# Kernel tuning notes

Hardware: AMD Instinct MI355X
Metric: run time of the kernel (lower is better)

The kernel has to match this reference:

```python
import jax, jax.numpy as jnp
import numpy as np

B, E, N, NREL, K, T, L = 8, 2000, 10000, 25, 16, 3, 32
TAU1 = 10.0

def _clip01(x):
    return jnp.clip(x, 0.0, 1.0)

def setup_inputs():
    key = jax.random.key(0)
    ks = jax.random.split(key, 10)
    ent = jax.random.randint(ks[0], (B,), 0, E)
    input_x = jnp.zeros((B, E), jnp.float32).at[jnp.arange(B), ent].set(1.0)
    tidx = jax.random.randint(ks[1], (E,), 0, K)
    type_mat = jnp.zeros((E, K), jnp.float32).at[jnp.arange(E), tidx].set(1.0)
    heads = jax.random.randint(ks[2], (N,), 0, E)
    tails = jax.random.randint(ks[3], (N,), 0, E)
    rels = jax.random.randint(ks[4], (N,), 0, NREL)
    e2triple = jnp.zeros((E, N), jnp.float32).at[heads, jnp.arange(N)].set(1.0)
    triple2e = jnp.zeros((N, E), jnp.float32).at[jnp.arange(N), tails].set(1.0)
    triple2r = jnp.zeros((N, NREL), jnp.float32).at[jnp.arange(N), rels].set(1.0)
    def ku(k, shape):
        fan_in = int(np.prod(shape[1:]))
        bnd = 1.0 / np.sqrt(fan_in)
        return jax.random.uniform(k, shape, jnp.float32, -bnd, bnd)
    w = ku(ks[5], (T, L, NREL))
    weight = ku(ks[6], (L, 1))
    h = jnp.ones((T, L, NREL - 1), jnp.float32)
    h_x = jnp.ones((L, NREL - 1), jnp.float32)
    h_type = ku(ks[7], (T, L, K))
    h_x_type = ku(ks[8], (L, K))
    alpha = jnp.ones((T, L), jnp.float32)
    beta = jnp.ones((T, L), jnp.float32)
    alpha_x = jnp.ones((L,), jnp.float32)
    beta_x = jnp.ones((L,), jnp.float32)
    return dict(input_x=input_x, type_mat=type_mat, e2triple=e2triple,
                triple2e=triple2e, triple2r=triple2r, w=w, weight=weight,
                h=h, h_x=h_x, h_type=h_type, h_x_type=h_x_type,
                alpha=alpha, beta=beta, alpha_x=alpha_x, beta_x=beta_x, flag=0)

def _forward(input_x, type_mat, e2triple, triple2e, triple2r, w, weight,
             h, h_x, h_type, h_x_type, alpha, beta, alpha_x, beta_x):
    # flag=False, is_training=False path of TCLMModel.forward
    Bb = input_x.shape[0]
    Nn, Ee = triple2e.shape
    Tt, Ll = alpha.shape
    nrel = w.shape[-1]
    half = (nrel - 1) // 2
    x_ori = input_x @ e2triple                      # [B,N]
    e2r = triple2e.T @ triple2r                     # [E,nrel]
    hidden_base = _clip01(e2r)[:, :-1]              # [E,nrel-1]
    hx_raw = _clip01(x_ori @ triple2r)              # [B,nrel]
    hidden_x_base = jnp.concatenate([hx_raw[:, half:-1], hx_raw[:, :half]], axis=-1)
    ax = _clip01(alpha_x / TAU1)
    bx = _clip01(beta_x / TAU1)
    gate_x = 1.0 - _clip01(ax + bx)                 # [L]
    hxp = _clip01(h_x / TAU1)                       # [L,nrel-1]
    hxtp = _clip01(h_x_type / TAU1)                 # [L,K]
    hidden_type_x = input_x @ (type_mat @ hxtp.T)   # [B,L]
    hx_lin = hidden_x_base @ hxp.T                  # [B,L]
    s = None
    for t in range(Tt):
        a = _clip01(alpha[t] / TAU1)                # [L]
        b = _clip01(beta[t] / TAU1)
        hp = _clip01(h[t] / TAU1)                   # [L,nrel-1]
        htp = _clip01(h_type[t] / TAU1)             # [L,K]
        hidden = _clip01(a[None] * (type_mat @ htp.T) + b[None] * (hidden_base @ hp.T))
        hidden = (hidden + (1.0 - _clip01(a + b))[None]).T        # [L,E]
        # note: original code uses alpha/beta (not alpha_x/beta_x) here; replicate
        hidden_x = _clip01(a[None] * hidden_type_x + b[None] * hx_lin) + gate_x[None]  # [B,L]
        w_probs = jax.nn.softmax(w[t], axis=-1)     # [L,nrel]
        srel = triple2r @ w_probs.T                 # [N,L]
        if t == 0:
            sc = x_ori[:, None, :] * srel.T[None]   # [B,L,N]
            s = (sc.reshape(-1, Nn) @ triple2e).reshape(Bb, Ll, Ee)
            s = s * hidden[None] * hidden_x[:, :, None]
        else:
            xprev = (s.reshape(-1, Ee) @ e2triple).reshape(Bb, Ll, Nn)
            sc = xprev * srel.T[None]               # [B,L,N]
            s = (sc.reshape(-1, Nn) @ triple2e).reshape(Bb, Ll, Ee)
            s = s * hidden[None]
    out = jnp.einsum('ble,lk->bek', s, jnp.tanh(weight))[..., 0]  # [B,E]
    return out

def reference(input_x, type_mat, e2triple, triple2e, triple2r, w, weight,
              h, h_x, h_type, h_x_type, alpha, beta, alpha_x, beta_x, flag):
    return _forward(input_x, type_mat, e2triple, triple2e, triple2r, w, weight,
                    h, h_x, h_type, h_x_type, alpha, beta, alpha_x, beta_x)
```

## Files before the change

### kernel.cpp

```cpp
#include <hip/hip_runtime.h>

#define B 8
#define E 2000
#define NTRI 10000
#define NRELS 25
#define KT 16
#define TT 3
#define LL 32
#define TAU1 10.0f
#define XBLK 2048
#define XTHR 256

__device__ __forceinline__ float clip01(float x) { return fminf(fmaxf(x, 0.0f), 1.0f); }

__device__ __forceinline__ void proc_e2t(float4 v, int i, unsigned int* packed) {
    if (v.x == 0.f && v.y == 0.f && v.z == 0.f && v.w == 0.f) return;
    int f = i * 4;
    float c[4] = {v.x, v.y, v.z, v.w};
#pragma unroll
    for (int k = 0; k < 4; k++)
        if (c[k] != 0.f) {
            int a = f + k;
            int head = a / NTRI;
            int j = a - head * NTRI;
            atomicOr(&packed[j], (unsigned int)head);
        }
}

__device__ __forceinline__ void proc_t2e(float4 v, int i, const float* __restrict__ t2r,
                                         unsigned int* packed, unsigned int* mask) {
    if (v.x == 0.f && v.y == 0.f && v.z == 0.f && v.w == 0.f) return;
    int f = i * 4;
    float c[4] = {v.x, v.y, v.z, v.w};
#pragma unroll
    for (int k = 0; k < 4; k++)
        if (c[k] != 0.f) {
            int a = f + k;
            int j = a / E;
            int tail = a - j * E;
            const float* row = t2r + j * NRELS;
            int r = 0;
            while (r < NRELS - 1 && row[r] == 0.f) r++;
            atomicOr(&packed[j], ((unsigned int)tail << 11) | ((unsigned int)r << 22));
            if (r < NRELS - 1) atomicOr(&mask[tail], 1u << r);
        }
}

__global__ void __launch_bounds__(XTHR) extract_all(
        const float4* __restrict__ e2t, const float4* __restrict__ t2e,
        const float* __restrict__ t2r, const float4* __restrict__ ix,
        const float4* __restrict__ tm,
        unsigned int* __restrict__ packed, unsigned int* __restrict__ mask,
        int* __restrict__ ent, int* __restrict__ tidx, float4* __restrict__ out4) {
    const int gtid = blockIdx.x * XTHR + threadIdx.x;
    const int gs = XBLK * XTHR;

    for (int i = gtid; i < B * E / 4; i += gs) {
        float4 v = ix[i];
        if (v.x != 0.f || v.y != 0.f || v.z != 0.f || v.w != 0.f) {
            int f = i * 4;
            float c[4] = {v.x, v.y, v.z, v.w};
#pragma unroll
            for (int k = 0; k < 4; k++)
                if (c[k] != 0.f) { int a = f + k; int b = a / E; ent[b] = a - b * E; }
        }
    }
    for (int i = gtid; i < E * KT / 4; i += gs) {
        float4 v = tm[i];
        if (v.x != 0.f || v.y != 0.f || v.z != 0.f || v.w != 0.f) {
            int f = i * 4;
            float c[4] = {v.x, v.y, v.z, v.w};
#pragma unroll
            for (int k = 0; k < 4; k++)
                if (c[k] != 0.f) { int a = f + k; int e = a / KT; tidx[e] = a - e * KT; }
        }
    }
    float4 z = make_float4(0.f, 0.f, 0.f, 0.f);
    for (int i = gtid; i < B * E / 4; i += gs) out4[i] = z;

    {
        const int n4 = E * NTRI / 4;
        for (int i0 = gtid; i0 < n4; i0 += gs * 4) {
            int i1 = i0 + gs, i2 = i0 + 2 * gs, i3 = i0 + 3 * gs;
            float4 v0 = e2t[i0];
            float4 v1 = (i1 < n4) ? e2t[i1] : z;
            float4 v2 = (i2 < n4) ? e2t[i2] : z;
            float4 v3 = (i3 < n4) ? e2t[i3] : z;
            proc_e2t(v0, i0, packed);
            proc_e2t(v1, i1, packed);
            proc_e2t(v2, i2, packed);
            proc_e2t(v3, i3, packed);
        }
    }
    {
        const int n4 = NTRI * E / 4;
        for (int i0 = gtid; i0 < n4; i0 += gs * 4) {
            int i1 = i0 + gs, i2 = i0 + 2 * gs, i3 = i0 + 3 * gs;
            float4 v0 = t2e[i0];
            float4 v1 = (i1 < n4) ? t2e[i1] : z;
            float4 v2 = (i2 < n4) ? t2e[i2] : z;
            float4 v3 = (i3 < n4) ? t2e[i3] : z;
            proc_t2e(v0, i0, t2r, packed, mask);
            proc_t2e(v1, i1, t2r, packed, mask);
            proc_t2e(v2, i2, t2r, packed, mask);
            proc_t2e(v3, i3, t2r, packed, mask);
        }
    }
}

__global__ void __launch_bounds__(512) mega_prop(
        const unsigned int* __restrict__ packed, const int* __restrict__ ent,
        const int* __restrict__ tidx, const unsigned int* __restrict__ mask,
        const float* __restrict__ w, const float* __restrict__ h,
        const float* __restrict__ h_type, const float* __restrict__ alpha,
        const float* __restrict__ beta, const float* __restrict__ h_x,
        const float* __restrict__ h_x_type, const float* __restrict__ alpha_x,
        const float* __restrict__ beta_x, const float* __restrict__ weight,
        float* __restrict__ out) {
    __shared__ float prev[E];
    __shared__ float acc[E];
    __shared__ unsigned int mask_s[E];
    __shared__ int tidx_s[E];
    __shared__ float wrow[NRELS];
    __shared__ float hp[NRELS - 1];
    __shared__ float htpL[KT];
    __shared__ unsigned int relflag;
    __shared__ float extra_s;

    const int NT = 512;
    const int blk = blockIdx.x, b = blk >> 5, l = blk & 31, tid = threadIdx.x;
    const int ent_b = ent[b];

    for (int e = tid; e < E; e += NT) {
        acc[e] = 0.f;
        mask_s[e] = mask[e];
        tidx_s[e] = tidx[e];
    }
    if (tid == 0) { relflag = 0u; extra_s = 1.f; }

    const uint4* p4 = (const uint4*)packed;

    for (int t = 0; t < TT; t++) {
        const int tl = t * LL + l;
        if (tid == 0) {
            const float* wr = w + tl * NRELS;
            float mx = wr[0];
            for (int r = 1; r < NRELS; r++) mx = fmaxf(mx, wr[r]);
            float ex[NRELS], s = 0.f;
            for (int r = 0; r < NRELS; r++) { ex[r] = expf(wr[r] - mx); s += ex[r]; }
            float inv = 1.f / s;
            for (int r = 0; r < NRELS; r++) wrow[r] = ex[r] * inv;
        }
        if (tid >= 64 && tid < 64 + NRELS - 1)
            hp[tid - 64] = clip01(h[tl * (NRELS - 1) + (tid - 64)] / TAU1);
        if (tid >= 128 && tid < 128 + KT)
            htpL[tid - 128] = clip01(h_type[tl * KT + (tid - 128)] / TAU1);
        __syncthreads();

        if (t == 0) {
            for (int i = tid; i < NTRI / 4; i += NT) {
                uint4 p = p4[i];
#pragma unroll
                for (int k = 0; k < 4; k++) {
                    unsigned int pk = (k == 0) ? p.x : (k == 1) ? p.y : (k == 2) ? p.z : p.w;
                    if ((int)(pk & 2047u) == ent_b) {
                        unsigned int r = pk >> 22;
                        int tail = (pk >> 11) & 2047;
                        atomicAdd(&acc[tail], wrow[r]);
                        atomicOr(&relflag, 1u << r);
                    }
                }
            }
        } else {
            for (int i = tid; i < NTRI / 4; i += NT) {
                uint4 p = p4[i];
#pragma unroll
                for (int k = 0; k < 4; k++) {
                    unsigned int pk = (k == 0) ? p.x : (k == 1) ? p.y : (k == 2) ? p.z : p.w;
                    float pv = prev[pk & 2047u];
                    if (pv != 0.f) {
                        unsigned int r = pk >> 22;
                        int tail = (pk >> 11) & 2047;
                        atomicAdd(&acc[tail], pv * wrow[r]);
                    }
                }
            }
        }
        __syncthreads();

        const float a = clip01(alpha[tl] / TAU1);
        const float bb = clip01(beta[tl] / TAU1);
        const float base = 1.f - clip01(a + bb);

        if (t == 0 && tid == 0) {
            unsigned int fl = relflag;
            float hxlin = 0.f;
            for (int i = 0; i < NRELS - 1; i++) {
                int pi = (i < 12) ? (12 + i) : (i - 12);
                if ((fl >> pi) & 1u) hxlin += clip01(h_x[l * (NRELS - 1) + i] / TAU1);
            }
            float htx = clip01(h_x_type[l * KT + tidx_s[ent_b]] / TAU1);
            float ax = clip01(alpha_x[l] / TAU1), bx = clip01(beta_x[l] / TAU1);
            extra_s = clip01(a * htx + bb * hxlin) + (1.f - clip01(ax + bx));
        }
        __syncthreads();

        const float extra = (t == 0) ? extra_s : 1.f;

        if (t < TT - 1) {
            for (int e = tid; e < E; e += NT) {
                unsigned int m = mask_s[e];
                float dot = 0.f;
#pragma unroll
                for (int i = 0; i < NRELS - 1; i++) dot += ((m >> i) & 1u) ? hp[i] : 0.f;
                float he = clip01(a * htpL[tidx_s[e]] + bb * dot) + base;
                prev[e] = acc[e] * he * extra;
                acc[e] = 0.f;
            }
        } else {
            float tw = tanhf(weight[l]);
            for (int e = tid; e < E; e += NT) {
                unsigned int m = mask_s[e];
                float dot = 0.f;
#pragma unroll
                for (int i = 0; i < NRELS - 1; i++) dot += ((m >> i) & 1u) ? hp[i] : 0.f;
                float he = clip01(a * htpL[tidx_s[e]] + bb * dot) + base;
                atomicAdd(&out[b * E + e], acc[e] * he * tw);
            }
        }
        __syncthreads();
    }
}

extern "C" void kernel_launch(void* const* d_in, const int* in_sizes, int n_in,
                              void* d_out, int out_size, void* d_ws, size_t ws_size,
                              hipStream_t stream) {
    const float* input_x  = (const float*)d_in[0];
    const float* type_mat = (const float*)d_in[1];
    const float* e2triple = (const float*)d_in[2];
    const float* triple2e = (const float*)d_in[3];
    const float* triple2r = (const float*)d_in[4];
    const float* w        = (const float*)d_in[5];
    const float* weight   = (const float*)d_in[6];
    const float* h        = (const float*)d_in[7];
    const float* h_x      = (const float*)d_in[8];
    const float* h_type   = (const float*)d_in[9];
    const float* h_x_type = (const float*)d_in[10];
    const float* alpha    = (const float*)d_in[11];
    const float* beta     = (const float*)d_in[12];
    const float* alpha_x  = (const float*)d_in[13];
    const float* beta_x   = (const float*)d_in[14];
    (void)in_sizes; (void)n_in; (void)out_size; (void)ws_size;

    char* ws = (char*)d_ws;
    size_t off = 0;
    auto alloc = [&](size_t bytes) -> void* {
        void* p = ws + off;
        off += (bytes + 255) & ~(size_t)255;
        return p;
    };
    unsigned int* packed = (unsigned int*)alloc(NTRI * sizeof(unsigned int));
    unsigned int* maskp  = (unsigned int*)alloc(E * sizeof(unsigned int));
    size_t zero_bytes = off;
    int* ent  = (int*)alloc(B * sizeof(int));
    int* tidx = (int*)alloc(E * sizeof(int));

    hipMemsetAsync(ws, 0, zero_bytes, stream);

    extract_all<<<XBLK, XTHR, 0, stream>>>((const float4*)e2triple, (const float4*)triple2e,
                                           triple2r, (const float4*)input_x,
                                           (const float4*)type_mat,
                                           packed, maskp, ent, tidx, (float4*)d_out);

    mega_prop<<<B * LL, 512, 0, stream>>>(packed, ent, tidx, maskp, w, h, h_type,
                                          alpha, beta, h_x, h_x_type, alpha_x, beta_x,
                                          weight, (float*)d_out);
}
```

Baseline: 244.0 us.

## Decouple relation extraction from triple2e scan and build type mask in shared memory

Relation indices are now read in a separate dense pass over triple2r instead of a dependent row scan per nonzero of triple2e. The per-entity relation mask is no longer built with global atomics in the extract kernel; each propagation block rebuilds it in shared memory during its first hop. The extract grid grows to 8192 blocks and the unroll-by-4 streaming loops become simple grid-stride loops. This trades a small redundant per-block shared-atomic mask build for removing serialized dependent loads and global atomics from the bandwidth-bound extraction.

```diff
diff --git a/kernel.cpp b/kernel.cpp
--- a/kernel.cpp
+++ b/kernel.cpp
@@ -8,49 +8,16 @@
 #define TT 3
 #define LL 32
 #define TAU1 10.0f
-#define XBLK 2048
+#define XBLK 8192
 #define XTHR 256
 
 __device__ __forceinline__ float clip01(float x) { return fminf(fmaxf(x, 0.0f), 1.0f); }
-
-__device__ __forceinline__ void proc_e2t(float4 v, int i, unsigned int* packed) {
-    if (v.x == 0.f && v.y == 0.f && v.z == 0.f && v.w == 0.f) return;
-    int f = i * 4;
-    float c[4] = {v.x, v.y, v.z, v.w};
-#pragma unroll
-    for (int k = 0; k < 4; k++)
-        if (c[k] != 0.f) {
-            int a = f + k;
-            int head = a / NTRI;
-            int j = a - head * NTRI;
-            atomicOr(&packed[j], (unsigned int)head);
-        }
-}
-
-__device__ __forceinline__ void proc_t2e(float4 v, int i, const float* __restrict__ t2r,
-                                         unsigned int* packed, unsigned int* mask) {
-    if (v.x == 0.f && v.y == 0.f && v.z == 0.f && v.w == 0.f) return;
-    int f = i * 4;
-    float c[4] = {v.x, v.y, v.z, v.w};
-#pragma unroll
-    for (int k = 0; k < 4; k++)
-        if (c[k] != 0.f) {
-            int a = f + k;
-            int j = a / E;
-            int tail = a - j * E;
-            const float* row = t2r + j * NRELS;
-            int r = 0;
-            while (r < NRELS - 1 && row[r] == 0.f) r++;
-            atomicOr(&packed[j], ((unsigned int)tail << 11) | ((unsigned int)r << 22));
-            if (r < NRELS - 1) atomicOr(&mask[tail], 1u << r);
-        }
-}
 
 __global__ void __launch_bounds__(XTHR) extract_all(
         const float4* __restrict__ e2t, const float4* __restrict__ t2e,
-        const float* __restrict__ t2r, const float4* __restrict__ ix,
+        const float4* __restrict__ t2r, const float4* __restrict__ ix,
         const float4* __restrict__ tm,
-        unsigned int* __restrict__ packed, unsigned int* __restrict__ mask,
+        unsigned int* __restrict__ packed,
         int* __restrict__ ent, int* __restrict__ tidx, float4* __restrict__ out4) {
     const int gtid = blockIdx.x * XTHR + threadIdx.x;
     const int gs = XBLK * XTHR;
@@ -78,39 +45,56 @@
     float4 z = make_float4(0.f, 0.f, 0.f, 0.f);
     for (int i = gtid; i < B * E / 4; i += gs) out4[i] = z;
 
-    {
-        const int n4 = E * NTRI / 4;
-        for (int i0 = gtid; i0 < n4; i0 += gs * 4) {
-            int i1 = i0 + gs, i2 = i0 + 2 * gs, i3 = i0 + 3 * gs;
-            float4 v0 = e2t[i0];
-            float4 v1 = (i1 < n4) ? e2t[i1] : z;
-            float4 v2 = (i2 < n4) ? e2t[i2] : z;
-            float4 v3 = (i3 < n4) ? e2t[i3] : z;
-            proc_e2t(v0, i0, packed);
-            proc_e2t(v1, i1, packed);
-            proc_e2t(v2, i2, packed);
-            proc_e2t(v3, i3, packed);
-        }
-    }
-    {
-        const int n4 = NTRI * E / 4;
-        for (int i0 = gtid; i0 < n4; i0 += gs * 4) {
-            int i1 = i0 + gs, i2 = i0 + 2 * gs, i3 = i0 + 3 * gs;
-            float4 v0 = t2e[i0];
-            float4 v1 = (i1 < n4) ? t2e[i1] : z;
-            float4 v2 = (i2 < n4) ? t2e[i2] : z;
-            float4 v3 = (i3 < n4) ? t2e[i3] : z;
-            proc_t2e(v0, i0, t2r, packed, mask);
-            proc_t2e(v1, i1, t2r, packed, mask);
-            proc_t2e(v2, i2, t2r, packed, mask);
-            proc_t2e(v3, i3, t2r, packed, mask);
+    for (int i = gtid; i < NTRI * NRELS / 4; i += gs) {
+        float4 v = t2r[i];
+        if (v.x != 0.f || v.y != 0.f || v.z != 0.f || v.w != 0.f) {
+            int f = i * 4;
+            float c[4] = {v.x, v.y, v.z, v.w};
+#pragma unroll
+            for (int k = 0; k < 4; k++)
+                if (c[k] != 0.f) {
+                    int a = f + k;
+                    int j = a / NRELS;
+                    unsigned int r = a - j * NRELS;
+                    atomicOr(&packed[j], r << 22);
+                }
+        }
+    }
+    for (int i = gtid; i < E * NTRI / 4; i += gs) {
+        float4 v = e2t[i];
+        if (v.x != 0.f || v.y != 0.f || v.z != 0.f || v.w != 0.f) {
+            int f = i * 4;
+            float c[4] = {v.x, v.y, v.z, v.w};
+#pragma unroll
+            for (int k = 0; k < 4; k++)
+                if (c[k] != 0.f) {
+                    int a = f + k;
+                    int head = a / NTRI;
+                    int j = a - head * NTRI;
+                    atomicOr(&packed[j], (unsigned int)head);
+                }
+        }
+    }
+    for (int i = gtid; i < NTRI * E / 4; i += gs) {
+        float4 v = t2e[i];
+        if (v.x != 0.f || v.y != 0.f || v.z != 0.f || v.w != 0.f) {
+            int f = i * 4;
+            float c[4] = {v.x, v.y, v.z, v.w};
+#pragma unroll
+            for (int k = 0; k < 4; k++)
+                if (c[k] != 0.f) {
+                    int a = f + k;
+                    int j = a / E;
+                    unsigned int tail = a - j * E;
+                    atomicOr(&packed[j], tail << 11);
+                }
         }
     }
 }
 
 __global__ void __launch_bounds__(512) mega_prop(
         const unsigned int* __restrict__ packed, const int* __restrict__ ent,
-        const int* __restrict__ tidx, const unsigned int* __restrict__ mask,
+        const int* __restrict__ tidx,
         const float* __restrict__ w, const float* __restrict__ h,
         const float* __restrict__ h_type, const float* __restrict__ alpha,
         const float* __restrict__ beta, const float* __restrict__ h_x,
@@ -133,7 +117,7 @@
 
     for (int e = tid; e < E; e += NT) {
         acc[e] = 0.f;
-        mask_s[e] = mask[e];
+        mask_s[e] = 0u;
         tidx_s[e] = tidx[e];
     }
     if (tid == 0) { relflag = 0u; extra_s = 1.f; }
@@ -163,9 +147,10 @@
 #pragma unroll
                 for (int k = 0; k < 4; k++) {
                     unsigned int pk = (k == 0) ? p.x : (k == 1) ? p.y : (k == 2) ? p.z : p.w;
+                    unsigned int r = pk >> 22;
+                    int tail = (pk >> 11) & 2047;
+                    if (r < NRELS - 1) atomicOr(&mask_s[tail], 1u << r);
                     if ((int)(pk & 2047u) == ent_b) {
-                        unsigned int r = pk >> 22;
-                        int tail = (pk >> 11) & 2047;
                         atomicAdd(&acc[tail], wrow[r]);
                         atomicOr(&relflag, 1u << r);
                     }
@@ -253,26 +238,18 @@
     (void)in_sizes; (void)n_in; (void)out_size; (void)ws_size;
 
     char* ws = (char*)d_ws;
-    size_t off = 0;
-    auto alloc = [&](size_t bytes) -> void* {
-        void* p = ws + off;
-        off += (bytes + 255) & ~(size_t)255;
-        return p;
-    };
-    unsigned int* packed = (unsigned int*)alloc(NTRI * sizeof(unsigned int));
-    unsigned int* maskp  = (unsigned int*)alloc(E * sizeof(unsigned int));
-    size_t zero_bytes = off;
-    int* ent  = (int*)alloc(B * sizeof(int));
-    int* tidx = (int*)alloc(E * sizeof(int));
-
-    hipMemsetAsync(ws, 0, zero_bytes, stream);
+    unsigned int* packed = (unsigned int*)ws;
+    int* ent  = (int*)(ws + ((NTRI * 4 + 255) & ~255));
+    int* tidx = ent + 64;
+
+    hipMemsetAsync(packed, 0, NTRI * sizeof(unsigned int), stream);
 
     extract_all<<<XBLK, XTHR, 0, stream>>>((const float4*)e2triple, (const float4*)triple2e,
-                                           triple2r, (const float4*)input_x,
+                                           (const float4*)triple2r, (const float4*)input_x,
                                            (const float4*)type_mat,
-                                           packed, maskp, ent, tidx, (float4*)d_out);
-
-    mega_prop<<<B * LL, 512, 0, stream>>>(packed, ent, tidx, maskp, w, h, h_type,
+                                           packed, ent, tidx, (float4*)d_out);
+
+    mega_prop<<<B * LL, 512, 0, stream>>>(packed, ent, tidx, w, h, h_type,
                                           alpha, beta, h_x, h_x_type, alpha_x, beta_x,
                                           weight, (float*)d_out);
 }
```

Result: faster. 223.2 us (-8.5%).
